# Optimization experiments

Hardware: AMD Instinct MI355X
Metric: run time of the kernel (lower is better)

## Reference

```python
import jax, jax.numpy as jnp
import numpy as np

IN_SIZE = 768
FC_SIZE = 3072
H = 12
ATT = IN_SIZE // H
EPS = 1e-5


def setup_inputs() -> dict:
    key = jax.random.key(0)
    ks = jax.random.split(key, 12)
    B, S = 4, 1024
    x = jax.random.normal(ks[0], (B, S, IN_SIZE), dtype=jnp.float32)
    mask = jax.random.randint(ks[1], (B, S, S), 0, 2, dtype=jnp.int32)
    s = 1.0 / np.sqrt(IN_SIZE)
    WQ = jax.random.normal(ks[2], (IN_SIZE, IN_SIZE), dtype=jnp.float32) * s
    WK = jax.random.normal(ks[3], (IN_SIZE, IN_SIZE), dtype=jnp.float32) * s
    WV = jax.random.normal(ks[4], (IN_SIZE, IN_SIZE), dtype=jnp.float32) * s
    Wfc = jax.random.normal(ks[5], (IN_SIZE, IN_SIZE), dtype=jnp.float32) * s
    W1 = jax.random.normal(ks[6], (IN_SIZE, FC_SIZE), dtype=jnp.float32) * s
    b1 = jnp.zeros((FC_SIZE,), dtype=jnp.float32)
    W2 = jax.random.normal(ks[7], (FC_SIZE, IN_SIZE), dtype=jnp.float32) / np.sqrt(FC_SIZE)
    b2 = jnp.zeros((IN_SIZE,), dtype=jnp.float32)
    g1 = jnp.ones((IN_SIZE,), dtype=jnp.float32)
    be1 = jnp.zeros((IN_SIZE,), dtype=jnp.float32)
    g2 = jnp.ones((IN_SIZE,), dtype=jnp.float32)
    be2 = jnp.zeros((IN_SIZE,), dtype=jnp.float32)
    return dict(x=x, mask=mask, WQ=WQ, WK=WK, WV=WV, Wfc=Wfc,
                W1=W1, b1=b1, W2=W2, b2=b2, g1=g1, be1=be1, g2=g2, be2=be2)


def _layernorm(x, g, b):
    mu = jnp.mean(x, axis=-1, keepdims=True)
    var = jnp.var(x, axis=-1, keepdims=True)
    return (x - mu) * jax.lax.rsqrt(var + EPS) * g + b


def reference(x, mask, WQ, WK, WV, Wfc, W1, b1, W2, b2, g1, be1, g2, be2):
    B, S, D = x.shape
    # NOTE: original code scales by sqrt(h), not sqrt(head_dim)
    scale = np.sqrt(H).astype(np.float32)
    Q = (x @ WQ).reshape(B, S, H, ATT).transpose(0, 2, 1, 3)  # [B,H,S,d]
    K = (x @ WK).reshape(B, S, H, ATT).transpose(0, 2, 1, 3)
    V = (x @ WV).reshape(B, S, H, ATT).transpose(0, 2, 1, 3)
    alpha = jnp.einsum('bhqd,bhkd->bhqk', Q, K) / scale
    alpha = jnp.where(mask[:, None, :, :] == 0, -1e9, alpha)
    alpha = jax.nn.softmax(alpha, axis=-1)
    att = jnp.einsum('bhqk,bhkd->bhqd', alpha, V)
    att = att.transpose(0, 2, 1, 3).reshape(B, S, D)
    att = att @ Wfc
    norm_att = _layernorm(att + x, g1, be1)
    lin = jax.nn.relu(norm_att @ W1 + b1) @ W2 + b2
    out = _layernorm(lin + norm_att, g2, be2)
    return out
```

## Files before the change

kernel.cpp:

```cpp
#include <hip/hip_runtime.h>
#include <stdint.h>

#define DMODEL 768
#define DFC    3072
#define NHEAD  12
#define DHEAD  64
#define BSZ    4
#define SEQ    1024
#define NTOK   (BSZ*SEQ)
#define QKVN   (3*DMODEL)

typedef unsigned short u16;
typedef unsigned int   u32;
typedef unsigned long long u64;
typedef __bf16 bf16_t;
typedef bf16_t bf16x8 __attribute__((ext_vector_type(8)));
typedef float  f32x4  __attribute__((ext_vector_type(4)));

__device__ __forceinline__ u16 f2b(float f) {
  u32 u = __builtin_bit_cast(u32, f);
  u = (u + 0x7FFFu + ((u >> 16) & 1u)) >> 16;
  return (u16)u;
}
__device__ __forceinline__ float b2f(u16 u) {
  return __builtin_bit_cast(float, (u32)u << 16);
}

__device__ __forceinline__ void gload_lds16(const void* g, void* l) {
  __builtin_amdgcn_global_load_lds(
      (const __attribute__((address_space(1))) void*)g,
      (__attribute__((address_space(3))) void*)l, 16, 0, 0);
}

__global__ __launch_bounds__(256) void mega_prep(
    const float* __restrict__ x, u16* __restrict__ XB,
    const float* __restrict__ WQ, const float* __restrict__ WK,
    const float* __restrict__ WV, const float* __restrict__ Wfc,
    const float* __restrict__ W1, const float* __restrict__ W2,
    u16* __restrict__ WQKVT, u16* __restrict__ WFCT,
    u16* __restrict__ W1T, u16* __restrict__ W2T,
    const int* __restrict__ mask, u64* __restrict__ MP) {
  __shared__ float tile[32][33];
  int bid = blockIdx.x, tid = threadIdx.x;

  if (bid < 3072) {
    int i = bid * 256 + tid;
    float4 v = ((const float4*)x)[i];
    ushort4 o;
    o.x = f2b(v.x); o.y = f2b(v.y); o.z = f2b(v.z); o.w = f2b(v.w);
    ((ushort4*)XB)[i] = o;
    return;
  }
  if (bid >= 9984) {
    int t = bid - 9984;
    int w = tid >> 6, lane = tid & 63;
    int idx = t * 4 + w;
    u64 bal = __ballot(mask[(size_t)idx * 64 + lane] != 0);
    if (lane == 0) MP[idx] = bal;
    return;
  }
  const float* in; u16* outp; int K, N, bx, by;
  if (bid < 5376) {
    int r = bid - 3072, which = r / 576, t = r % 576;
    in = which == 0 ? WQ : which == 1 ? WK : which == 2 ? WV : Wfc;
    outp = which < 3 ? WQKVT + (size_t)which * DMODEL * DMODEL : WFCT;
    K = DMODEL; N = DMODEL; bx = (t % 24) * 32; by = (t / 24) * 32;
  } else if (bid < 7680) {
    int t = bid - 5376;
    in = W1; outp = W1T; K = DMODEL; N = DFC;
    bx = (t % 96) * 32; by = (t / 96) * 32;
  } else {
    int t = bid - 7680;
    in = W2; outp = W2T; K = DFC; N = DMODEL;
    bx = (t % 24) * 32; by = (t / 24) * 32;
  }
  int tx = tid & 31, ty = tid >> 5;
#pragma unroll
  for (int i = 0; i < 4; ++i)
    tile[ty + i * 8][tx] = in[(size_t)(by + ty + i * 8) * N + bx + tx];
  __syncthreads();
#pragma unroll
  for (int i = 0; i < 4; ++i)
    outp[(size_t)(bx + ty + i * 8) * K + by + tx] = f2b(tile[tx][ty + i * 8]);
}

__global__ __launch_bounds__(256) void build_vt(const u16* __restrict__ QKVM,
                                                u16* __restrict__ VT) {
  __shared__ u16 t[64][72];
  int st = blockIdx.x, h = blockIdx.y, b = blockIdx.z;
  int tid = threadIdx.x;
  const u16* src = QKVM + ((size_t)(b * SEQ + st * 64)) * QKVN + 2 * DMODEL + h * DHEAD;
#pragma unroll
  for (int p = 0; p < 2; ++p) {
    int s = (p * 256 + tid) >> 3, c8 = tid & 7;
    *(uint4*)&t[s][c8 * 8] = *(const uint4*)&src[(size_t)s * QKVN + c8 * 8];
  }
  __syncthreads();
  u16* dst = VT + ((size_t)(b * NHEAD + h) * 64) * SEQ + st * 64;
#pragma unroll
  for (int p = 0; p < 2; ++p) {
    int d = (p * 256 + tid) >> 3, s8 = tid & 7;
    union { uint4 v; u16 s[8]; } o;
#pragma unroll
    for (int j = 0; j < 8; ++j) o.s[j] = t[s8 * 8 + j][d];
    *(uint4*)&dst[(size_t)d * SEQ + s8 * 8] = o.v;
  }
}

template <int MODE, int SPLIT>
__global__ __launch_bounds__(256) void gemm_bt(const u16* __restrict__ A,
                                               const u16* __restrict__ Bt,
                                               void* __restrict__ Cout,
                                               const float* __restrict__ bias,
                                               u16* __restrict__ pA, u16* __restrict__ pB,
                                               int M, int N, int K) {
  __shared__ __align__(16) u16 ldsA[2][128 * 32];
  __shared__ __align__(16) u16 ldsB[2][128 * 32];
  int tid = threadIdx.x;
  int lane = tid & 63, l15 = lane & 15, g = lane >> 4;
  int w = tid >> 6, wm = w >> 1, wn = w & 1;
  int m0 = blockIdx.y * 128, n0 = blockIdx.x * 128;
  int KS = K / SPLIT;
  int k0 = blockIdx.z * KS;
  int NT = KS >> 5;

  f32x4 acc[4][4];
#pragma unroll
  for (int i = 0; i < 4; ++i)
#pragma unroll
    for (int j = 0; j < 4; ++j) acc[i][j] = (f32x4){0.f, 0.f, 0.f, 0.f};

  const u16* gabase = A + (size_t)m0 * K + k0;
  const u16* gbbase = Bt + (size_t)n0 * K + k0;
  int wbase = tid & ~63;
  int lswz = (lane & 3) ^ ((lane >> 3) & 3);

  auto stage = [&](int kt, int buf) {
#pragma unroll
    for (int p = 0; p < 2; ++p) {
      int c = p * 256 + tid;
      int row = c >> 2;
      size_t goff = (size_t)row * K + kt * 32 + lswz * 8;
      gload_lds16(gabase + goff, &ldsA[buf][(p * 256 + wbase) * 8]);
      gload_lds16(gbbase + goff, &ldsB[buf][(p * 256 + wbase) * 8]);
    }
  };

  int rswz = (l15 >> 1) & 3;

  stage(0, 0);
  __syncthreads();
  for (int kt = 0; kt < NT; ++kt) {
    int cur = kt & 1;
    if (kt + 1 < NT) stage(kt + 1, cur ^ 1);
    bf16x8 af[4], bfr[4];
#pragma unroll
    for (int i = 0; i < 4; ++i) {
      af[i]  = *(const bf16x8*)&ldsA[cur][(wm * 64 + i * 16 + l15) * 32 + (g ^ rswz) * 8];
      bfr[i] = *(const bf16x8*)&ldsB[cur][(wn * 64 + i * 16 + l15) * 32 + (g ^ rswz) * 8];
    }
#pragma unroll
    for (int i = 0; i < 4; ++i)
#pragma unroll
      for (int j = 0; j < 4; ++j)
        acc[i][j] = __builtin_amdgcn_mfma_f32_16x16x32_bf16(af[i], bfr[j], acc[i][j], 0, 0, 0);
    __syncthreads();
  }

  u16* pdst = nullptr;
  if (MODE == 5)
    pdst = ((blockIdx.z & 2) ? pB : pA) + (size_t)(blockIdx.z & 1) * M * N;
#pragma unroll
  for (int i = 0; i < 4; ++i) {
#pragma unroll
    for (int j = 0; j < 4; ++j) {
#pragma unroll
      for (int r = 0; r < 4; ++r) {
        int row = m0 + wm * 64 + i * 16 + g * 4 + r;
        int col = n0 + wn * 64 + j * 16 + l15;
        float v = acc[i][j][r];
        if (MODE == 2) {
          v += bias[col];
          v = v > 0.f ? v : 0.f;
        }
        if (MODE == 0 || MODE == 2)
          ((u16*)Cout)[(size_t)row * N + col] = f2b(v);
        else if (MODE == 4)
          ((float*)Cout)[(size_t)blockIdx.z * M * N + (size_t)row * N + col] = v;
        else
          pdst[(size_t)row * N + col] = f2b(v);
      }
    }
  }
}

__global__ __launch_bounds__(256) void attn_kernel(const u16* __restrict__ QKVM,
                                                   const u16* __restrict__ VT,
                                                   const u64* __restrict__ MP,
                                                   u16* __restrict__ Om) {
  __shared__ __align__(16) u16 ldsK[2][64 * 64];
  __shared__ __align__(16) u16 ldsV[2][64 * 64];
  __shared__ __align__(16) u16 P_lds[4][16][72];

  int qt = blockIdx.x, h = blockIdx.y, b = blockIdx.z;
  int tid = threadIdx.x, w = tid >> 6, lane = tid & 63;
  int l15 = lane & 15, g = lane >> 4, l7 = lane & 7;
  int q0 = qt * 64 + w * 16;

  const u16* Qb = QKVM + (size_t)(b * SEQ) * QKVN + h * DHEAD;
  const u16* Kb = QKVM + (size_t)(b * SEQ) * QKVN + DMODEL + h * DHEAD;
  const u16* Vb = VT + (size_t)(b * NHEAD + h) * 64 * SEQ;

  bf16x8 qf[2];
  qf[0] = *(const bf16x8*)&Qb[(size_t)(q0 + l15) * QKVN + g * 8];
  qf[1] = *(const bf16x8*)&Qb[(size_t)(q0 + l15) * QKVN + 32 + g * 8];

  int r8 = lane >> 3, sl = lane & 7, slg = sl ^ r8;

  auto stage = [&](int kt, int buf) {
#pragma unroll
    for (int p = 0; p < 2; ++p) {
      int c = p * 4 + w;
      int row = c * 8 + r8;
      gload_lds16(Kb + (size_t)(kt * 64 + row) * QKVN + slg * 8, &ldsK[buf][c * 512]);
      gload_lds16(Vb + (size_t)row * SEQ + kt * 64 + slg * 8, &ldsV[buf][c * 512]);
    }
  };

  f32x4 acc[4];
  float ps[4];
#pragma unroll
  for (int d = 0; d < 4; ++d) acc[d] = (f32x4){0.f, 0.f, 0.f, 0.f};
#pragma unroll
  for (int r = 0; r < 4; ++r) ps[r] = 0.f;

  const float SC2 = 0.41650835f;

  stage(0, 0);
  __syncthreads();

  for (int kt = 0; kt < SEQ / 64; ++kt) {
    int cur = kt & 1;
    if (kt + 1 < SEQ / 64) stage(kt + 1, cur ^ 1);

    u64 mw[4];
#pragma unroll
    for (int r = 0; r < 4; ++r)
      mw[r] = MP[((size_t)(b * SEQ + q0 + g * 4 + r) << 4) | kt];

    f32x4 s[4];
#pragma unroll
    for (int fn = 0; fn < 4; ++fn) s[fn] = (f32x4){0.f, 0.f, 0.f, 0.f};
#pragma unroll
    for (int kf = 0; kf < 2; ++kf)
#pragma unroll
      for (int fn = 0; fn < 4; ++fn) {
        bf16x8 kfrag = *(const bf16x8*)((const char*)&ldsK[cur][0] +
                         (fn * 16 + l15) * 128 + (((kf * 4 + g) ^ l7) << 4));
        s[fn] = __builtin_amdgcn_mfma_f32_16x16x32_bf16(qf[kf], kfrag, s[fn], 0, 0, 0);
      }

#pragma unroll
    for (int fn = 0; fn < 4; ++fn) {
      u32 hv[4];
#pragma unroll
      for (int r = 0; r < 4; ++r)
        hv[r] = (fn & 2) ? (u32)(mw[r] >> 32) : (u32)mw[r];
      u32 bitpos = ((fn & 1) << 4) + l15;
#pragma unroll
      for (int r = 0; r < 4; ++r) {
        float pe = __builtin_amdgcn_exp2f(s[fn][r] * SC2);
        float p = ((hv[r] >> bitpos) & 1u) ? pe : 0.f;
        ps[r] += p;
        P_lds[w][g * 4 + r][fn * 16 + l15] = f2b(p);
      }
    }

#pragma unroll
    for (int kf2 = 0; kf2 < 2; ++kf2) {
      bf16x8 pf = *(const bf16x8*)((const char*)&P_lds[w][0][0] +
                    l15 * 144 + (kf2 * 32 + g * 8) * 2);
#pragma unroll
      for (int d = 0; d < 4; ++d) {
        bf16x8 vf = *(const bf16x8*)((const char*)&ldsV[cur][0] +
                      (d * 16 + l15) * 128 + (((kf2 * 4 + g) ^ l7) << 4));
        acc[d] = __builtin_amdgcn_mfma_f32_16x16x32_bf16(pf, vf, acc[d], 0, 0, 0);
      }
    }
    __syncthreads();
  }

#pragma unroll
  for (int r = 0; r < 4; ++r) {
#pragma unroll
    for (int off = 1; off < 16; off <<= 1) ps[r] += __shfl_xor(ps[r], off);
    ps[r] = 1.f / ps[r];
  }
#pragma unroll
  for (int d = 0; d < 4; ++d)
#pragma unroll
    for (int r = 0; r < 4; ++r) {
      float o = acc[d][r] * ps[r];
      Om[(size_t)(b * SEQ + q0 + g * 4 + r) * DMODEL + h * DHEAD + d * 16 + l15] = f2b(o);
    }
}

__global__ __launch_bounds__(256) void ln_sum2(const float* __restrict__ parts,
                                               const float* __restrict__ res,
                                               const float* __restrict__ gam,
                                               const float* __restrict__ bet,
                                               float* __restrict__ of,
                                               u16* __restrict__ ob) {
  int w = threadIdx.x >> 6, lane = threadIdx.x & 63;
  int row = blockIdx.x * 4 + w;
  const float* p0 = parts + (size_t)row * DMODEL;
  const float* p1 = parts + (size_t)NTOK * DMODEL + (size_t)row * DMODEL;
  const float* pr = res + (size_t)row * DMODEL;
  float4 v[3];
  float s = 0.f, s2 = 0.f;
#pragma unroll
  for (int j = 0; j < 3; ++j) {
    int c = lane * 4 + j * 256;
    float4 a = *(const float4*)&p0[c];
    float4 b = *(const float4*)&p1[c];
    float4 r = *(const float4*)&pr[c];
    float4 t = {a.x + b.x + r.x, a.y + b.y + r.y, a.z + b.z + r.z, a.w + b.w + r.w};
    v[j] = t;
    s += t.x + t.y + t.z + t.w;
    s2 += t.x * t.x + t.y * t.y + t.z * t.z + t.w * t.w;
  }
#pragma unroll
  for (int off = 32; off; off >>= 1) {
    s += __shfl_xor(s, off);
    s2 += __shfl_xor(s2, off);
  }
  float mu = s * (1.f / DMODEL);
  float var = s2 * (1.f / DMODEL) - mu * mu;
  float rs = rsqrtf(var + 1e-5f);
#pragma unroll
  for (int j = 0; j < 3; ++j) {
    int c = lane * 4 + j * 256;
    float4 gm = *(const float4*)&gam[c];
    float4 bt = *(const float4*)&bet[c];
    float4 o = {(v[j].x - mu) * rs * gm.x + bt.x, (v[j].y - mu) * rs * gm.y + bt.y,
                (v[j].z - mu) * rs * gm.z + bt.z, (v[j].w - mu) * rs * gm.w + bt.w};
    *(float4*)&of[(size_t)row * DMODEL + c] = o;
    ushort4 ub = {f2b(o.x), f2b(o.y), f2b(o.z), f2b(o.w)};
    *(ushort4*)&ob[(size_t)row * DMODEL + c] = ub;
  }
}

__global__ __launch_bounds__(256) void ln_sum4(const u16* __restrict__ pA,
                                               const u16* __restrict__ pB,
                                               const float* __restrict__ res,
                                               const float* __restrict__ badd,
                                               const float* __restrict__ gam,
                                               const float* __restrict__ bet,
                                               float* __restrict__ of) {
  int w = threadIdx.x >> 6, lane = threadIdx.x & 63;
  int row = blockIdx.x * 4 + w;
  size_t ro = (size_t)row * DMODEL;
  const size_t PS = (size_t)NTOK * DMODEL;
  float4 v[3];
  float s = 0.f, s2 = 0.f;
#pragma unroll
  for (int j = 0; j < 3; ++j) {
    int c = lane * 4 + j * 256;
    ushort4 u0 = *(const ushort4*)&pA[ro + c];
    ushort4 u1 = *(const ushort4*)&pA[PS + ro + c];
    ushort4 u2 = *(const ushort4*)&pB[ro + c];
    ushort4 u3 = *(const ushort4*)&pB[PS + ro + c];
    float4 r = *(const float4*)&res[ro + c];
    float4 bb = *(const float4*)&badd[c];
    float4 t = {b2f(u0.x) + b2f(u1.x) + b2f(u2.x) + b2f(u3.x) + r.x + bb.x,
                b2f(u0.y) + b2f(u1.y) + b2f(u2.y) + b2f(u3.y) + r.y + bb.y,
                b2f(u0.z) + b2f(u1.z) + b2f(u2.z) + b2f(u3.z) + r.z + bb.z,
                b2f(u0.w) + b2f(u1.w) + b2f(u2.w) + b2f(u3.w) + r.w + bb.w};
    v[j] = t;
    s += t.x + t.y + t.z + t.w;
    s2 += t.x * t.x + t.y * t.y + t.z * t.z + t.w * t.w;
  }
#pragma unroll
  for (int off = 32; off; off >>= 1) {
    s += __shfl_xor(s, off);
    s2 += __shfl_xor(s2, off);
  }
  float mu = s * (1.f / DMODEL);
  float var = s2 * (1.f / DMODEL) - mu * mu;
  float rs = rsqrtf(var + 1e-5f);
#pragma unroll
  for (int j = 0; j < 3; ++j) {
    int c = lane * 4 + j * 256;
    float4 gm = *(const float4*)&gam[c];
    float4 bt = *(const float4*)&bet[c];
    float4 o = {(v[j].x - mu) * rs * gm.x + bt.x, (v[j].y - mu) * rs * gm.y + bt.y,
                (v[j].z - mu) * rs * gm.z + bt.z, (v[j].w - mu) * rs * gm.w + bt.w};
    *(float4*)&of[ro + c] = o;
  }
}

extern "C" void kernel_launch(void* const* d_in, const int* in_sizes, int n_in,
                              void* d_out, int out_size, void* d_ws, size_t ws_size,
                              hipStream_t stream) {
  const float* x   = (const float*)d_in[0];
  const int*   msk = (const int*)d_in[1];
  const float* WQ  = (const float*)d_in[2];
  const float* WK  = (const float*)d_in[3];
  const float* WV  = (const float*)d_in[4];
  const float* Wfc = (const float*)d_in[5];
  const float* W1  = (const float*)d_in[6];
  const float* b1  = (const float*)d_in[7];
  const float* W2  = (const float*)d_in[8];
  const float* b2  = (const float*)d_in[9];
  const float* g1  = (const float*)d_in[10];
  const float* be1 = (const float*)d_in[11];
  const float* g2  = (const float*)d_in[12];
  const float* be2 = (const float*)d_in[13];
  float* out = (float*)d_out;

  char* ws = (char*)d_ws;
  u16*  XB    = (u16*)(ws + 0);
  u16*  WQKVT = (u16*)(ws + 6291456);
  u16*  WFCT  = (u16*)(ws + 9830400);
  u16*  W1T   = (u16*)(ws + 11010048);
  u16*  W2T   = (u16*)(ws + 15728640);
  u16*  QKVM  = (u16*)(ws + 20447232);
  u16*  VT    = (u16*)(ws + 39321600);
  u64*  MP    = (u64*)(ws + 45613056);
  float* NAF  = (float*)(ws + 46137344);
  u16*  NAB   = (u16*)(ws + 58720256);
  u16*   ATTO    = XB;
  float* PROJP   = (float*)QKVM;
  u16*   HMID    = QKVM;
  u16*   LINPA   = (u16*)(ws + 0);
  u16*   LINPB   = (u16*)(ws + 58720256);

  mega_prep<<<dim3(26368), dim3(256), 0, stream>>>(x, XB, WQ, WK, WV, Wfc, W1, W2,
                                                   WQKVT, WFCT, W1T, W2T, msk, MP);

  gemm_bt<0, 1><<<dim3(QKVN / 128, NTOK / 128, 1), dim3(256), 0, stream>>>(
      XB, WQKVT, QKVM, nullptr, nullptr, nullptr, NTOK, QKVN, DMODEL);
  build_vt<<<dim3(SEQ / 64, NHEAD, BSZ), dim3(256), 0, stream>>>(QKVM, VT);
  attn_kernel<<<dim3(SEQ / 64, NHEAD, BSZ), dim3(256), 0, stream>>>(QKVM, VT, MP, ATTO);

  gemm_bt<4, 2><<<dim3(DMODEL / 128, NTOK / 128, 2), dim3(256), 0, stream>>>(
      ATTO, WFCT, PROJP, nullptr, nullptr, nullptr, NTOK, DMODEL, DMODEL);
  ln_sum2<<<dim3(NTOK / 4), dim3(256), 0, stream>>>(PROJP, x, g1, be1, NAF, NAB);

  gemm_bt<2, 1><<<dim3(DFC / 128, NTOK / 128, 1), dim3(256), 0, stream>>>(
      NAB, W1T, HMID, b1, nullptr, nullptr, NTOK, DFC, DMODEL);
  gemm_bt<5, 4><<<dim3(DMODEL / 128, NTOK / 128, 4), dim3(256), 0, stream>>>(
      HMID, W2T, nullptr, nullptr, LINPA, LINPB, NTOK, DMODEL, DFC);
  ln_sum4<<<dim3(NTOK / 4), dim3(256), 0, stream>>>(LINPA, LINPB, NAF, b2, g2, be2, out);

  (void)in_sizes; (void)n_in; (void)out_size; (void)ws_size;
}
```

Before: 280.3 us.

## Rewrite attention with 32x32 MFMA, register-resident P, and XCD-aware block remap

The attention kernel moves to two 32-row waves per block using 32x32x16 bf16 MFMA. It computes S^T so the probabilities stay in registers and are reshuffled with permlane32_swap, which removes the P round trip through LDS. Attention and GEMM block IDs are remapped so neighbouring tiles land on the same XCD for better L2 reuse, and f2b now uses the hardware bf16 conversion. The risks are lower occupancy per block, more registers held by the 16-wide accumulators, and the extra index arithmetic for the remap.

```diff
diff --git a/kernel.cpp b/kernel.cpp
--- a/kernel.cpp
+++ b/kernel.cpp
@@ -15,15 +15,21 @@
 typedef unsigned long long u64;
 typedef __bf16 bf16_t;
 typedef bf16_t bf16x8 __attribute__((ext_vector_type(8)));
+typedef bf16_t bf16x2 __attribute__((ext_vector_type(2)));
 typedef float  f32x4  __attribute__((ext_vector_type(4)));
+typedef float  f32x16 __attribute__((ext_vector_type(16)));
+typedef u32    u32x2  __attribute__((ext_vector_type(2)));
 
 __device__ __forceinline__ u16 f2b(float f) {
-  u32 u = __builtin_bit_cast(u32, f);
-  u = (u + 0x7FFFu + ((u >> 16) & 1u)) >> 16;
-  return (u16)u;
+  __bf16 h = (__bf16)f;
+  return __builtin_bit_cast(u16, h);
 }
 __device__ __forceinline__ float b2f(u16 u) {
   return __builtin_bit_cast(float, (u32)u << 16);
+}
+__device__ __forceinline__ u32 pk2(float a, float b) {
+  bf16x2 t = {(__bf16)a, (__bf16)b};
+  return __builtin_bit_cast(u32, t);
 }
 
 __device__ __forceinline__ void gload_lds16(const void* g, void* l) {
@@ -119,7 +125,13 @@
   int tid = threadIdx.x;
   int lane = tid & 63, l15 = lane & 15, g = lane >> 4;
   int w = tid >> 6, wm = w >> 1, wn = w & 1;
-  int m0 = blockIdx.y * 128, n0 = blockIdx.x * 128;
+
+  int gx = gridDim.x;
+  int bid = blockIdx.y * gx + blockIdx.x;
+  int nwg = gx * gridDim.y;
+  int wgid = ((nwg & 7) == 0) ? ((bid & 7) * (nwg >> 3) + (bid >> 3)) : bid;
+  int m0 = (wgid / gx) * 128, n0 = (wgid % gx) * 128;
+
   int KS = K / SPLIT;
   int k0 = blockIdx.z * KS;
   int NT = KS >> 5;
@@ -194,45 +206,47 @@
   }
 }
 
-__global__ __launch_bounds__(256) void attn_kernel(const u16* __restrict__ QKVM,
+__global__ __launch_bounds__(128) void attn_kernel(const u16* __restrict__ QKVM,
                                                    const u16* __restrict__ VT,
                                                    const u64* __restrict__ MP,
                                                    u16* __restrict__ Om) {
   __shared__ __align__(16) u16 ldsK[2][64 * 64];
   __shared__ __align__(16) u16 ldsV[2][64 * 64];
-  __shared__ __align__(16) u16 P_lds[4][16][72];
-
-  int qt = blockIdx.x, h = blockIdx.y, b = blockIdx.z;
+
+  int bid = blockIdx.x;
+  int logical = (bid & 7) * 96 + (bid >> 3);
+  int qt = logical & 15, hb = logical >> 4;
+  int h = hb % NHEAD, b = hb / NHEAD;
+
   int tid = threadIdx.x, w = tid >> 6, lane = tid & 63;
-  int l15 = lane & 15, g = lane >> 4, l7 = lane & 7;
-  int q0 = qt * 64 + w * 16;
+  int l31 = lane & 31, hi = lane >> 5, l7 = l31 & 7;
+  int q0w = qt * 64 + w * 32;
 
   const u16* Qb = QKVM + (size_t)(b * SEQ) * QKVN + h * DHEAD;
   const u16* Kb = QKVM + (size_t)(b * SEQ) * QKVN + DMODEL + h * DHEAD;
   const u16* Vb = VT + (size_t)(b * NHEAD + h) * 64 * SEQ;
 
-  bf16x8 qf[2];
-  qf[0] = *(const bf16x8*)&Qb[(size_t)(q0 + l15) * QKVN + g * 8];
-  qf[1] = *(const bf16x8*)&Qb[(size_t)(q0 + l15) * QKVN + 32 + g * 8];
+  bf16x8 qf[4];
+#pragma unroll
+  for (int dt = 0; dt < 4; ++dt)
+    qf[dt] = *(const bf16x8*)&Qb[(size_t)(q0w + l31) * QKVN + dt * 16 + hi * 8];
 
   int r8 = lane >> 3, sl = lane & 7, slg = sl ^ r8;
-
   auto stage = [&](int kt, int buf) {
 #pragma unroll
-    for (int p = 0; p < 2; ++p) {
-      int c = p * 4 + w;
-      int row = c * 8 + r8;
-      gload_lds16(Kb + (size_t)(kt * 64 + row) * QKVN + slg * 8, &ldsK[buf][c * 512]);
-      gload_lds16(Vb + (size_t)row * SEQ + kt * 64 + slg * 8, &ldsV[buf][c * 512]);
+    for (int p = 0; p < 4; ++p) {
+      int row = p * 16 + w * 8 + r8;
+      gload_lds16(Kb + (size_t)(kt * 64 + row) * QKVN + slg * 8, &ldsK[buf][(p * 16 + w * 8) * 64]);
+      gload_lds16(Vb + (size_t)row * SEQ + kt * 64 + slg * 8, &ldsV[buf][(p * 16 + w * 8) * 64]);
     }
   };
 
-  f32x4 acc[4];
-  float ps[4];
-#pragma unroll
-  for (int d = 0; d < 4; ++d) acc[d] = (f32x4){0.f, 0.f, 0.f, 0.f};
-#pragma unroll
-  for (int r = 0; r < 4; ++r) ps[r] = 0.f;
+  f32x16 acc[2];
+#pragma unroll
+  for (int d2 = 0; d2 < 2; ++d2)
+#pragma unroll
+    for (int r = 0; r < 16; ++r) acc[d2][r] = 0.f;
+  float ps = 0.f;
 
   const float SC2 = 0.41650835f;
 
@@ -243,65 +257,67 @@
     int cur = kt & 1;
     if (kt + 1 < SEQ / 64) stage(kt + 1, cur ^ 1);
 
-    u64 mw[4];
-#pragma unroll
-    for (int r = 0; r < 4; ++r)
-      mw[r] = MP[((size_t)(b * SEQ + q0 + g * 4 + r) << 4) | kt];
-
-    f32x4 s[4];
-#pragma unroll
-    for (int fn = 0; fn < 4; ++fn) s[fn] = (f32x4){0.f, 0.f, 0.f, 0.f};
-#pragma unroll
-    for (int kf = 0; kf < 2; ++kf)
-#pragma unroll
-      for (int fn = 0; fn < 4; ++fn) {
-        bf16x8 kfrag = *(const bf16x8*)((const char*)&ldsK[cur][0] +
-                         (fn * 16 + l15) * 128 + (((kf * 4 + g) ^ l7) << 4));
-        s[fn] = __builtin_amdgcn_mfma_f32_16x16x32_bf16(qf[kf], kfrag, s[fn], 0, 0, 0);
+    u64 mw = MP[((size_t)(b * SEQ + q0w + l31) << 4) | kt];
+
+#pragma unroll
+    for (int kk = 0; kk < 2; ++kk) {
+      f32x16 sacc;
+#pragma unroll
+      for (int r = 0; r < 16; ++r) sacc[r] = 0.f;
+#pragma unroll
+      for (int dt = 0; dt < 4; ++dt) {
+        bf16x8 kf = *(const bf16x8*)((const char*)&ldsK[cur][0] +
+                      (kk * 32 + l31) * 128 + (((dt * 2 + hi) ^ l7) << 4));
+        sacc = __builtin_amdgcn_mfma_f32_32x32x16_bf16(kf, qf[dt], sacc, 0, 0, 0);
       }
 
-#pragma unroll
-    for (int fn = 0; fn < 4; ++fn) {
-      u32 hv[4];
-#pragma unroll
-      for (int r = 0; r < 4; ++r)
-        hv[r] = (fn & 2) ? (u32)(mw[r] >> 32) : (u32)mw[r];
-      u32 bitpos = ((fn & 1) << 4) + l15;
-#pragma unroll
-      for (int r = 0; r < 4; ++r) {
-        float pe = __builtin_amdgcn_exp2f(s[fn][r] * SC2);
-        float p = ((hv[r] >> bitpos) & 1u) ? pe : 0.f;
-        ps[r] += p;
-        P_lds[w][g * 4 + r][fn * 16 + l15] = f2b(p);
+      u32 mh = (u32)(mw >> (kk * 32 + 4 * hi));
+      float p[16];
+#pragma unroll
+      for (int r = 0; r < 16; ++r) {
+        float pe = __builtin_amdgcn_exp2f(sacc[r] * SC2);
+        p[r] = ((mh >> ((r & 3) + 8 * (r >> 2))) & 1u) ? pe : 0.f;
+        ps += p[r];
       }
-    }
-
-#pragma unroll
-    for (int kf2 = 0; kf2 < 2; ++kf2) {
-      bf16x8 pf = *(const bf16x8*)((const char*)&P_lds[w][0][0] +
-                    l15 * 144 + (kf2 * 32 + g * 8) * 2);
-#pragma unroll
-      for (int d = 0; d < 4; ++d) {
-        bf16x8 vf = *(const bf16x8*)((const char*)&ldsV[cur][0] +
-                      (d * 16 + l15) * 128 + (((kf2 * 4 + g) ^ l7) << 4));
-        acc[d] = __builtin_amdgcn_mfma_f32_16x16x32_bf16(pf, vf, acc[d], 0, 0, 0);
+
+#pragma unroll
+      for (int kt2 = 0; kt2 < 2; ++kt2) {
+        u32 w0 = pk2(p[kt2 * 8 + 0], p[kt2 * 8 + 1]);
+        u32 w1 = pk2(p[kt2 * 8 + 2], p[kt2 * 8 + 3]);
+        u32 w2 = pk2(p[kt2 * 8 + 4], p[kt2 * 8 + 5]);
+        u32 w3 = pk2(p[kt2 * 8 + 6], p[kt2 * 8 + 7]);
+        u32x2 rA = __builtin_amdgcn_permlane32_swap(w0, w2, false, false);
+        u32x2 rB = __builtin_amdgcn_permlane32_swap(w1, w3, false, false);
+        union { u32 u[4]; bf16x8 v; } pa;
+        pa.u[0] = rA[0];
+        pa.u[1] = rB[0];
+        pa.u[2] = rA[1];
+        pa.u[3] = rB[1];
+#pragma unroll
+        for (int d2 = 0; d2 < 2; ++d2) {
+          bf16x8 vf = *(const bf16x8*)((const char*)&ldsV[cur][0] +
+                        (d2 * 32 + l31) * 128 + (((kk * 4 + kt2 * 2 + hi) ^ l7) << 4));
+          acc[d2] = __builtin_amdgcn_mfma_f32_32x32x16_bf16(pa.v, vf, acc[d2], 0, 0, 0);
+        }
       }
     }
     __syncthreads();
   }
 
-#pragma unroll
-  for (int r = 0; r < 4; ++r) {
-#pragma unroll
-    for (int off = 1; off < 16; off <<= 1) ps[r] += __shfl_xor(ps[r], off);
-    ps[r] = 1.f / ps[r];
-  }
-#pragma unroll
-  for (int d = 0; d < 4; ++d)
-#pragma unroll
-    for (int r = 0; r < 4; ++r) {
-      float o = acc[d][r] * ps[r];
-      Om[(size_t)(b * SEQ + q0 + g * 4 + r) * DMODEL + h * DHEAD + d * 16 + l15] = f2b(o);
+  float pst = ps + __shfl_xor(ps, 32);
+  float invp = 1.f / pst;
+  float sc[16];
+#pragma unroll
+  for (int r = 0; r < 16; ++r)
+    sc[r] = __shfl(invp, (r & 3) + 8 * (r >> 2) + 4 * hi);
+
+#pragma unroll
+  for (int d2 = 0; d2 < 2; ++d2)
+#pragma unroll
+    for (int r = 0; r < 16; ++r) {
+      int ql = (r & 3) + 8 * (r >> 2) + 4 * hi;
+      Om[(size_t)(b * SEQ + q0w + ql) * DMODEL + h * DHEAD + d2 * 32 + l31] =
+          f2b(acc[d2][r] * sc[r]);
     }
 }
 
@@ -441,7 +457,7 @@
   gemm_bt<0, 1><<<dim3(QKVN / 128, NTOK / 128, 1), dim3(256), 0, stream>>>(
       XB, WQKVT, QKVM, nullptr, nullptr, nullptr, NTOK, QKVN, DMODEL);
   build_vt<<<dim3(SEQ / 64, NHEAD, BSZ), dim3(256), 0, stream>>>(QKVM, VT);
-  attn_kernel<<<dim3(SEQ / 64, NHEAD, BSZ), dim3(256), 0, stream>>>(QKVM, VT, MP, ATTO);
+  attn_kernel<<<dim3(BSZ * NHEAD * (SEQ / 64)), dim3(128), 0, stream>>>(QKVM, VT, MP, ATTO);
 
   gemm_bt<4, 2><<<dim3(DMODEL / 128, NTOK / 128, 2), dim3(256), 0, stream>>>(
       ATTO, WFCT, PROJP, nullptr, nullptr, nullptr, NTOK, DMODEL, DMODEL);
```

Result: no change. 275.8 us (-1.6%).
